# Optimization experiments

Measured on AMD Instinct MI355X. Metric: run time of the kernel, lower is better.

## Reference

```python
import jax, jax.numpy as jnp
import numpy as np


def setup_inputs() -> dict:
    key = jax.random.key(0)
    k1, k2 = jax.random.split(key)
    shape = (4096, 16384)  # d_model x d_ff weight matrix, 64M elements
    weight = jax.random.normal(k1, shape, dtype=jnp.float32)
    mask_weights = jax.random.normal(k2, shape, dtype=jnp.float32)
    return {"weight": weight, "mask_weights": mask_weights, "masking_percent": 0.5}


def reference(weight, mask_weights, masking_percent):
    # torch: topk(mask_weights.flat, k=int((1-p)*N), largest=False) -> zero those
    # positions in a clone of weight.
    flat_mask = mask_weights.reshape(-1)
    n = flat_mask.shape[0]
    k = int((1.0 - masking_percent) * n)  # static python int (p is a python float)
    # bottom-k of mask_weights == top-k of its negation
    _, bottomk_idx = jax.lax.top_k(-flat_mask, k)
    masked = weight.reshape(-1).at[bottomk_idx].set(0.0)
    return masked.reshape(weight.shape)
```

## Files before the change

kernel.cpp:

```cpp
#include <hip/hip_runtime.h>

#define HIST_BITS 12
#define NBINS (1 << HIST_BITS)
#define KEY_SHIFT (32 - HIST_BITS)
#define REP 4

typedef float fx4 __attribute__((ext_vector_type(4)));

struct Ctrl {
    long long k;
    long long r1;
    int b1;
    unsigned counter;
};

__device__ __forceinline__ unsigned fkey(float f) {
    unsigned u = __float_as_uint(f);
    return (u & 0x80000000u) ? ~u : (u | 0x80000000u);
}

__global__ void k_zero(unsigned* __restrict__ hist, Ctrl* __restrict__ ctrl) {
    int i = blockIdx.x * blockDim.x + threadIdx.x;
    if (i < NBINS) hist[i] = 0;
    if (i == 0) {
        ctrl->k = 0; ctrl->r1 = 0; ctrl->b1 = -1; ctrl->counter = 0;
    }
}

__global__ void __launch_bounds__(1024)
k_hist(const float* __restrict__ mask, long long n, unsigned* __restrict__ ghist) {
    __shared__ unsigned sh[NBINS * REP];
    for (int i = threadIdx.x; i < NBINS * REP; i += blockDim.x) sh[i] = 0;
    __syncthreads();

    const unsigned r = threadIdx.x & (REP - 1);
    const long long n4 = n >> 2;
    const fx4* m4 = (const fx4*)mask;
    const long long B = blockDim.x;
    const long long per = (n4 + gridDim.x - 1) / gridDim.x;
    const long long s0 = (long long)blockIdx.x * per;
    const long long e = (s0 + per < n4) ? s0 + per : n4;

    long long i = s0 + threadIdx.x;
    for (; i + 3 * B < e; i += 4 * B) {
        fx4 a = m4[i];
        fx4 b = m4[i + B];
        fx4 c = m4[i + 2 * B];
        fx4 d = m4[i + 3 * B];
        atomicAdd(&sh[(fkey(a.x) >> KEY_SHIFT) * REP + r], 1u);
        atomicAdd(&sh[(fkey(a.y) >> KEY_SHIFT) * REP + r], 1u);
        atomicAdd(&sh[(fkey(a.z) >> KEY_SHIFT) * REP + r], 1u);
        atomicAdd(&sh[(fkey(a.w) >> KEY_SHIFT) * REP + r], 1u);
        atomicAdd(&sh[(fkey(b.x) >> KEY_SHIFT) * REP + r], 1u);
        atomicAdd(&sh[(fkey(b.y) >> KEY_SHIFT) * REP + r], 1u);
        atomicAdd(&sh[(fkey(b.z) >> KEY_SHIFT) * REP + r], 1u);
        atomicAdd(&sh[(fkey(b.w) >> KEY_SHIFT) * REP + r], 1u);
        atomicAdd(&sh[(fkey(c.x) >> KEY_SHIFT) * REP + r], 1u);
        atomicAdd(&sh[(fkey(c.y) >> KEY_SHIFT) * REP + r], 1u);
        atomicAdd(&sh[(fkey(c.z) >> KEY_SHIFT) * REP + r], 1u);
        atomicAdd(&sh[(fkey(c.w) >> KEY_SHIFT) * REP + r], 1u);
        atomicAdd(&sh[(fkey(d.x) >> KEY_SHIFT) * REP + r], 1u);
        atomicAdd(&sh[(fkey(d.y) >> KEY_SHIFT) * REP + r], 1u);
        atomicAdd(&sh[(fkey(d.z) >> KEY_SHIFT) * REP + r], 1u);
        atomicAdd(&sh[(fkey(d.w) >> KEY_SHIFT) * REP + r], 1u);
    }
    for (; i < e; i += B) {
        fx4 a = m4[i];
        atomicAdd(&sh[(fkey(a.x) >> KEY_SHIFT) * REP + r], 1u);
        atomicAdd(&sh[(fkey(a.y) >> KEY_SHIFT) * REP + r], 1u);
        atomicAdd(&sh[(fkey(a.z) >> KEY_SHIFT) * REP + r], 1u);
        atomicAdd(&sh[(fkey(a.w) >> KEY_SHIFT) * REP + r], 1u);
    }
    if (blockIdx.x == 0 && threadIdx.x == 0) {
        for (long long t = n4 * 4; t < n; ++t)
            atomicAdd(&ghist[fkey(mask[t]) >> KEY_SHIFT], 1u);
    }
    __syncthreads();
    for (int b = threadIdx.x; b < NBINS; b += blockDim.x) {
        unsigned s = sh[b * REP] + sh[b * REP + 1] + sh[b * REP + 2] + sh[b * REP + 3];
        if (s) atomicAdd(&ghist[b], s);
    }
}

__global__ void k_scan(const unsigned* __restrict__ ghist, Ctrl* __restrict__ ctrl,
                       const float* __restrict__ p_ptr, long long n) {
    __shared__ long long part[256];
    __shared__ long long kk_sh;
    const int t = threadIdx.x;
    if (t == 0) {
        double p = (double)p_ptr[0];
        long long k = (long long)((1.0 - p) * (double)n);
        if (k < 0) k = 0;
        if (k > n) k = n;
        kk_sh = k;
        ctrl->k = k;
        ctrl->b1 = -1;
        ctrl->r1 = 0;
    }
    __syncthreads();
    const long long k = kk_sh;

    const int per = NBINS / 256;
    long long s = 0;
    for (int i = 0; i < per; ++i) s += (long long)ghist[t * per + i];
    part[t] = s;
    __syncthreads();
    for (int off = 1; off < 256; off <<= 1) {
        long long add = (t >= off) ? part[t - off] : 0;
        __syncthreads();
        part[t] += add;
        __syncthreads();
    }
    if (k >= 1) {
        long long incl = part[t];
        long long excl = incl - s;
        if (excl < k && k <= incl) {
            long long cum = excl;
            for (int i = 0; i < per; ++i) {
                long long c = (long long)ghist[t * per + i];
                if (cum < k && k <= cum + c) {
                    ctrl->b1 = t * per + i;
                    ctrl->r1 = k - cum;
                    break;
                }
                cum += c;
            }
        }
    }
}

__device__ __forceinline__ void cand4(unsigned k0, unsigned k1, unsigned k2, unsigned k3,
                                      unsigned base, unsigned b1u,
                                      Ctrl* ctrl, uint2* list, unsigned cap) {
    if ((k0 >> KEY_SHIFT) == b1u) { unsigned p = atomicAdd(&ctrl->counter, 1u); if (p < cap) list[p] = make_uint2(k0, base + 0); }
    if ((k1 >> KEY_SHIFT) == b1u) { unsigned p = atomicAdd(&ctrl->counter, 1u); if (p < cap) list[p] = make_uint2(k1, base + 1); }
    if ((k2 >> KEY_SHIFT) == b1u) { unsigned p = atomicAdd(&ctrl->counter, 1u); if (p < cap) list[p] = make_uint2(k2, base + 2); }
    if ((k3 >> KEY_SHIFT) == b1u) { unsigned p = atomicAdd(&ctrl->counter, 1u); if (p < cap) list[p] = make_uint2(k3, base + 3); }
}

__global__ void __launch_bounds__(256)
k_apply(const float* __restrict__ w, const float* __restrict__ mask,
        float* __restrict__ out, long long n,
        Ctrl* __restrict__ ctrl, uint2* __restrict__ list, unsigned cap) {
    const int b1 = ctrl->b1;
    const unsigned b1u = (unsigned)b1;
    const unsigned lo = (b1 <= 0) ? 0u : ((unsigned)b1 << KEY_SHIFT);
    const long long n4 = n >> 2;
    const fx4* m4 = (const fx4*)mask;
    const fx4* w4 = (const fx4*)w;
    fx4* o4 = (fx4*)out;
    const long long B = blockDim.x;
    const long long per = (n4 + gridDim.x - 1) / gridDim.x;
    const long long s0 = (long long)blockIdx.x * per;
    const long long e = (s0 + per < n4) ? s0 + per : n4;

    long long i = s0 + threadIdx.x;
    for (; i + 3 * B < e; i += 4 * B) {
        fx4 m0 = m4[i];
        fx4 m1 = m4[i + B];
        fx4 m2 = m4[i + 2 * B];
        fx4 m3 = m4[i + 3 * B];
        fx4 w0 = __builtin_nontemporal_load(&w4[i]);
        fx4 w1 = __builtin_nontemporal_load(&w4[i + B]);
        fx4 w2 = __builtin_nontemporal_load(&w4[i + 2 * B]);
        fx4 w3 = __builtin_nontemporal_load(&w4[i + 3 * B]);
        unsigned k00 = fkey(m0.x), k01 = fkey(m0.y), k02 = fkey(m0.z), k03 = fkey(m0.w);
        unsigned k10 = fkey(m1.x), k11 = fkey(m1.y), k12 = fkey(m1.z), k13 = fkey(m1.w);
        unsigned k20 = fkey(m2.x), k21 = fkey(m2.y), k22 = fkey(m2.z), k23 = fkey(m2.w);
        unsigned k30 = fkey(m3.x), k31 = fkey(m3.y), k32 = fkey(m3.z), k33 = fkey(m3.w);
        fx4 o0, o1, o2, o3;
        o0.x = (k00 >= lo) ? w0.x : 0.0f;  o0.y = (k01 >= lo) ? w0.y : 0.0f;
        o0.z = (k02 >= lo) ? w0.z : 0.0f;  o0.w = (k03 >= lo) ? w0.w : 0.0f;
        o1.x = (k10 >= lo) ? w1.x : 0.0f;  o1.y = (k11 >= lo) ? w1.y : 0.0f;
        o1.z = (k12 >= lo) ? w1.z : 0.0f;  o1.w = (k13 >= lo) ? w1.w : 0.0f;
        o2.x = (k20 >= lo) ? w2.x : 0.0f;  o2.y = (k21 >= lo) ? w2.y : 0.0f;
        o2.z = (k22 >= lo) ? w2.z : 0.0f;  o2.w = (k23 >= lo) ? w2.w : 0.0f;
        o3.x = (k30 >= lo) ? w3.x : 0.0f;  o3.y = (k31 >= lo) ? w3.y : 0.0f;
        o3.z = (k32 >= lo) ? w3.z : 0.0f;  o3.w = (k33 >= lo) ? w3.w : 0.0f;
        __builtin_nontemporal_store(o0, &o4[i]);
        __builtin_nontemporal_store(o1, &o4[i + B]);
        __builtin_nontemporal_store(o2, &o4[i + 2 * B]);
        __builtin_nontemporal_store(o3, &o4[i + 3 * B]);
        bool anyc = ((k00 >> KEY_SHIFT) == b1u) | ((k01 >> KEY_SHIFT) == b1u) |
                    ((k02 >> KEY_SHIFT) == b1u) | ((k03 >> KEY_SHIFT) == b1u) |
                    ((k10 >> KEY_SHIFT) == b1u) | ((k11 >> KEY_SHIFT) == b1u) |
                    ((k12 >> KEY_SHIFT) == b1u) | ((k13 >> KEY_SHIFT) == b1u) |
                    ((k20 >> KEY_SHIFT) == b1u) | ((k21 >> KEY_SHIFT) == b1u) |
                    ((k22 >> KEY_SHIFT) == b1u) | ((k23 >> KEY_SHIFT) == b1u) |
                    ((k30 >> KEY_SHIFT) == b1u) | ((k31 >> KEY_SHIFT) == b1u) |
                    ((k32 >> KEY_SHIFT) == b1u) | ((k33 >> KEY_SHIFT) == b1u);
        if (__any(anyc)) {
            cand4(k00, k01, k02, k03, (unsigned)(i * 4), b1u, ctrl, list, cap);
            cand4(k10, k11, k12, k13, (unsigned)((i + B) * 4), b1u, ctrl, list, cap);
            cand4(k20, k21, k22, k23, (unsigned)((i + 2 * B) * 4), b1u, ctrl, list, cap);
            cand4(k30, k31, k32, k33, (unsigned)((i + 3 * B) * 4), b1u, ctrl, list, cap);
        }
    }
    for (; i < e; i += B) {
        fx4 m0 = m4[i];
        fx4 w0 = __builtin_nontemporal_load(&w4[i]);
        unsigned k00 = fkey(m0.x), k01 = fkey(m0.y), k02 = fkey(m0.z), k03 = fkey(m0.w);
        fx4 o0;
        o0.x = (k00 >= lo) ? w0.x : 0.0f;  o0.y = (k01 >= lo) ? w0.y : 0.0f;
        o0.z = (k02 >= lo) ? w0.z : 0.0f;  o0.w = (k03 >= lo) ? w0.w : 0.0f;
        __builtin_nontemporal_store(o0, &o4[i]);
        bool anyc = ((k00 >> KEY_SHIFT) == b1u) | ((k01 >> KEY_SHIFT) == b1u) |
                    ((k02 >> KEY_SHIFT) == b1u) | ((k03 >> KEY_SHIFT) == b1u);
        if (__any(anyc))
            cand4(k00, k01, k02, k03, (unsigned)(i * 4), b1u, ctrl, list, cap);
    }
    if (blockIdx.x == 0 && threadIdx.x == 0) {
        for (long long t = n4 * 4; t < n; ++t) {
            unsigned key = fkey(mask[t]);
            out[t] = (key >= lo) ? w[t] : 0.0f;
            if ((key >> KEY_SHIFT) == b1u) {
                unsigned p = atomicAdd(&ctrl->counter, 1u);
                if (p < cap) list[p] = make_uint2(key, (unsigned)t);
            }
        }
    }
}

__global__ void k_fix(float* __restrict__ out, const Ctrl* __restrict__ ctrl,
                      const uint2* __restrict__ list, unsigned cap) {
    __shared__ uint2 ch[1024];
    unsigned nc = ctrl->counter;
    if (nc > cap) nc = cap;
    const long long r1 = ctrl->r1;
    if (ctrl->b1 < 0 || r1 <= 0) return;

    for (unsigned jb = 0; jb < nc; jb += blockDim.x) {
        unsigned j = jb + threadIdx.x;
        bool act = (j < nc);
        unsigned kj = 0, ij = 0;
        if (act) { uint2 e = list[j]; kj = e.x; ij = e.y; }
        long long rank = 0;
        for (unsigned cb = 0; cb < nc; cb += 1024) {
            unsigned mlen = nc - cb; if (mlen > 1024) mlen = 1024;
            for (unsigned u = threadIdx.x; u < mlen; u += blockDim.x) ch[u] = list[cb + u];
            __syncthreads();
            if (act) {
                for (unsigned u = 0; u < mlen; ++u) {
                    uint2 e = ch[u];
                    rank += (long long)((e.x < kj) || (e.x == kj && e.y < ij));
                }
            }
            __syncthreads();
        }
        if (act && rank < r1) out[ij] = 0.0f;
    }
}

extern "C" void kernel_launch(void* const* d_in, const int* in_sizes, int n_in,
                              void* d_out, int out_size, void* d_ws, size_t ws_size,
                              hipStream_t stream) {
    const float* weight = (const float*)d_in[0];
    const float* maskw  = (const float*)d_in[1];
    const float* pptr   = (const float*)d_in[2];
    float* out = (float*)d_out;
    const long long n = (long long)in_sizes[0];

    unsigned char* ws = (unsigned char*)d_ws;
    unsigned* hist = (unsigned*)ws;
    Ctrl* ctrl = (Ctrl*)(ws + 16384);
    uint2* list = (uint2*)(ws + 16416);
    size_t cap_sz = (ws_size > 16416) ? (ws_size - 16416) / sizeof(uint2) : 0;
    unsigned cap = (unsigned)(cap_sz > (size_t)(1u << 20) ? (1u << 20) : cap_sz);

    k_zero<<<(NBINS + 255) / 256, 256, 0, stream>>>(hist, ctrl);
    k_hist<<<512, 1024, 0, stream>>>(maskw, n, hist);
    k_scan<<<1, 256, 0, stream>>>(hist, ctrl, pptr, n);
    k_apply<<<2048, 256, 0, stream>>>(weight, maskw, out, n, ctrl, list, cap);
    k_fix<<<1, 256, 0, stream>>>(out, ctrl, list, cap);
}
```

Baseline: 185.1 us.

## Fuse histogram, scan and apply into one persistent kernel with grid barrier

Merges the histogram, threshold scan and masking kernels into a single 512x1024 kernel. The last-arriving block does the prefix scan while the other blocks spin on a flag, then every block applies the mask to the same slice it histogrammed. This is meant to cut kernel launch gaps and to make the second mask read come from cache. In exchange it depends on all blocks being co-resident, which risks a deadlock or timeout, and the single scanning block sits on the critical path while every other block waits.

Measured after the change: 381.6 us. 106% more time.

```diff
diff --git a/kernel.cpp b/kernel.cpp
--- a/kernel.cpp
+++ b/kernel.cpp
@@ -4,6 +4,8 @@
 #define NBINS (1 << HIST_BITS)
 #define KEY_SHIFT (32 - HIST_BITS)
 #define REP 4
+#define GRID 512
+#define BLK 1024
 
 typedef float fx4 __attribute__((ext_vector_type(4)));
 
@@ -12,6 +14,8 @@
     long long r1;
     int b1;
     unsigned counter;
+    unsigned arrive;
+    unsigned flag;
 };
 
 __device__ __forceinline__ unsigned fkey(float f) {
@@ -23,138 +27,144 @@
     int i = blockIdx.x * blockDim.x + threadIdx.x;
     if (i < NBINS) hist[i] = 0;
     if (i == 0) {
-        ctrl->k = 0; ctrl->r1 = 0; ctrl->b1 = -1; ctrl->counter = 0;
-    }
-}
-
-__global__ void __launch_bounds__(1024)
-k_hist(const float* __restrict__ mask, long long n, unsigned* __restrict__ ghist) {
+        ctrl->k = 0; ctrl->r1 = 0; ctrl->b1 = -1;
+        ctrl->counter = 0; ctrl->arrive = 0; ctrl->flag = 0;
+    }
+}
+
+__global__ void __launch_bounds__(BLK, 8)
+k_fused(const float* __restrict__ w, const float* __restrict__ mask,
+        float* __restrict__ out, long long n, const float* __restrict__ p_ptr,
+        unsigned* __restrict__ ghist, Ctrl* __restrict__ ctrl,
+        uint2* __restrict__ list, unsigned cap) {
     __shared__ unsigned sh[NBINS * REP];
-    for (int i = threadIdx.x; i < NBINS * REP; i += blockDim.x) sh[i] = 0;
-    __syncthreads();
-
-    const unsigned r = threadIdx.x & (REP - 1);
+    __shared__ int s_last;
+    __shared__ int sb1;
+
+    const int tid = threadIdx.x;
+    if (tid == 0) s_last = 0;
+    for (int i = tid; i < NBINS * REP; i += BLK) sh[i] = 0;
+    __syncthreads();
+
     const long long n4 = n >> 2;
     const fx4* m4 = (const fx4*)mask;
-    const long long B = blockDim.x;
+    const long long B = BLK;
     const long long per = (n4 + gridDim.x - 1) / gridDim.x;
     const long long s0 = (long long)blockIdx.x * per;
     const long long e = (s0 + per < n4) ? s0 + per : n4;
 
-    long long i = s0 + threadIdx.x;
-    for (; i + 3 * B < e; i += 4 * B) {
-        fx4 a = m4[i];
-        fx4 b = m4[i + B];
-        fx4 c = m4[i + 2 * B];
-        fx4 d = m4[i + 3 * B];
-        atomicAdd(&sh[(fkey(a.x) >> KEY_SHIFT) * REP + r], 1u);
-        atomicAdd(&sh[(fkey(a.y) >> KEY_SHIFT) * REP + r], 1u);
-        atomicAdd(&sh[(fkey(a.z) >> KEY_SHIFT) * REP + r], 1u);
-        atomicAdd(&sh[(fkey(a.w) >> KEY_SHIFT) * REP + r], 1u);
-        atomicAdd(&sh[(fkey(b.x) >> KEY_SHIFT) * REP + r], 1u);
-        atomicAdd(&sh[(fkey(b.y) >> KEY_SHIFT) * REP + r], 1u);
-        atomicAdd(&sh[(fkey(b.z) >> KEY_SHIFT) * REP + r], 1u);
-        atomicAdd(&sh[(fkey(b.w) >> KEY_SHIFT) * REP + r], 1u);
-        atomicAdd(&sh[(fkey(c.x) >> KEY_SHIFT) * REP + r], 1u);
-        atomicAdd(&sh[(fkey(c.y) >> KEY_SHIFT) * REP + r], 1u);
-        atomicAdd(&sh[(fkey(c.z) >> KEY_SHIFT) * REP + r], 1u);
-        atomicAdd(&sh[(fkey(c.w) >> KEY_SHIFT) * REP + r], 1u);
-        atomicAdd(&sh[(fkey(d.x) >> KEY_SHIFT) * REP + r], 1u);
-        atomicAdd(&sh[(fkey(d.y) >> KEY_SHIFT) * REP + r], 1u);
-        atomicAdd(&sh[(fkey(d.z) >> KEY_SHIFT) * REP + r], 1u);
-        atomicAdd(&sh[(fkey(d.w) >> KEY_SHIFT) * REP + r], 1u);
-    }
-    for (; i < e; i += B) {
-        fx4 a = m4[i];
-        atomicAdd(&sh[(fkey(a.x) >> KEY_SHIFT) * REP + r], 1u);
-        atomicAdd(&sh[(fkey(a.y) >> KEY_SHIFT) * REP + r], 1u);
-        atomicAdd(&sh[(fkey(a.z) >> KEY_SHIFT) * REP + r], 1u);
-        atomicAdd(&sh[(fkey(a.w) >> KEY_SHIFT) * REP + r], 1u);
-    }
-    if (blockIdx.x == 0 && threadIdx.x == 0) {
-        for (long long t = n4 * 4; t < n; ++t)
-            atomicAdd(&ghist[fkey(mask[t]) >> KEY_SHIFT], 1u);
-    }
-    __syncthreads();
-    for (int b = threadIdx.x; b < NBINS; b += blockDim.x) {
+    {
+        const unsigned r = tid & (REP - 1);
+        long long i = s0 + tid;
+        for (; i + 3 * B < e; i += 4 * B) {
+            fx4 a = m4[i];
+            fx4 b = m4[i + B];
+            fx4 c = m4[i + 2 * B];
+            fx4 d = m4[i + 3 * B];
+            atomicAdd(&sh[(fkey(a.x) >> KEY_SHIFT) * REP + r], 1u);
+            atomicAdd(&sh[(fkey(a.y) >> KEY_SHIFT) * REP + r], 1u);
+            atomicAdd(&sh[(fkey(a.z) >> KEY_SHIFT) * REP + r], 1u);
+            atomicAdd(&sh[(fkey(a.w) >> KEY_SHIFT) * REP + r], 1u);
+            atomicAdd(&sh[(fkey(b.x) >> KEY_SHIFT) * REP + r], 1u);
+            atomicAdd(&sh[(fkey(b.y) >> KEY_SHIFT) * REP + r], 1u);
+            atomicAdd(&sh[(fkey(b.z) >> KEY_SHIFT) * REP + r], 1u);
+            atomicAdd(&sh[(fkey(b.w) >> KEY_SHIFT) * REP + r], 1u);
+            atomicAdd(&sh[(fkey(c.x) >> KEY_SHIFT) * REP + r], 1u);
+            atomicAdd(&sh[(fkey(c.y) >> KEY_SHIFT) * REP + r], 1u);
+            atomicAdd(&sh[(fkey(c.z) >> KEY_SHIFT) * REP + r], 1u);
+            atomicAdd(&sh[(fkey(c.w) >> KEY_SHIFT) * REP + r], 1u);
+            atomicAdd(&sh[(fkey(d.x) >> KEY_SHIFT) * REP + r], 1u);
+            atomicAdd(&sh[(fkey(d.y) >> KEY_SHIFT) * REP + r], 1u);
+            atomicAdd(&sh[(fkey(d.z) >> KEY_SHIFT) * REP + r], 1u);
+            atomicAdd(&sh[(fkey(d.w) >> KEY_SHIFT) * REP + r], 1u);
+        }
+        for (; i < e; i += B) {
+            fx4 a = m4[i];
+            atomicAdd(&sh[(fkey(a.x) >> KEY_SHIFT) * REP + r], 1u);
+            atomicAdd(&sh[(fkey(a.y) >> KEY_SHIFT) * REP + r], 1u);
+            atomicAdd(&sh[(fkey(a.z) >> KEY_SHIFT) * REP + r], 1u);
+            atomicAdd(&sh[(fkey(a.w) >> KEY_SHIFT) * REP + r], 1u);
+        }
+        if (blockIdx.x == 0 && tid == 0) {
+            for (long long t = n4 * 4; t < n; ++t)
+                atomicAdd(&ghist[fkey(mask[t]) >> KEY_SHIFT], 1u);
+        }
+    }
+    __syncthreads();
+    for (int b = tid; b < NBINS; b += BLK) {
         unsigned s = sh[b * REP] + sh[b * REP + 1] + sh[b * REP + 2] + sh[b * REP + 3];
         if (s) atomicAdd(&ghist[b], s);
     }
-}
-
-__global__ void k_scan(const unsigned* __restrict__ ghist, Ctrl* __restrict__ ctrl,
-                       const float* __restrict__ p_ptr, long long n) {
-    __shared__ long long part[256];
-    __shared__ long long kk_sh;
-    const int t = threadIdx.x;
-    if (t == 0) {
+    __threadfence();
+    __syncthreads();
+
+    if (tid == 0) {
+        unsigned old = atomicAdd(&ctrl->arrive, 1u);
+        if (old == gridDim.x - 1) s_last = 1;
+    }
+    __syncthreads();
+
+    if (s_last) {
+        long long* part = (long long*)sh;
         double p = (double)p_ptr[0];
-        long long k = (long long)((1.0 - p) * (double)n);
-        if (k < 0) k = 0;
-        if (k > n) k = n;
-        kk_sh = k;
-        ctrl->k = k;
-        ctrl->b1 = -1;
-        ctrl->r1 = 0;
-    }
-    __syncthreads();
-    const long long k = kk_sh;
-
-    const int per = NBINS / 256;
-    long long s = 0;
-    for (int i = 0; i < per; ++i) s += (long long)ghist[t * per + i];
-    part[t] = s;
-    __syncthreads();
-    for (int off = 1; off < 256; off <<= 1) {
-        long long add = (t >= off) ? part[t - off] : 0;
+        long long kk = (long long)((1.0 - p) * (double)n);
+        if (kk < 0) kk = 0;
+        if (kk > n) kk = n;
+        const int pern = NBINS / BLK;
+        unsigned c0 = __hip_atomic_load(&ghist[tid * pern + 0], __ATOMIC_RELAXED, __HIP_MEMORY_SCOPE_AGENT);
+        unsigned c1 = __hip_atomic_load(&ghist[tid * pern + 1], __ATOMIC_RELAXED, __HIP_MEMORY_SCOPE_AGENT);
+        unsigned c2 = __hip_atomic_load(&ghist[tid * pern + 2], __ATOMIC_RELAXED, __HIP_MEMORY_SCOPE_AGENT);
+        unsigned c3 = __hip_atomic_load(&ghist[tid * pern + 3], __ATOMIC_RELAXED, __HIP_MEMORY_SCOPE_AGENT);
+        long long s = (long long)c0 + c1 + c2 + c3;
+        part[tid] = s;
         __syncthreads();
-        part[t] += add;
+        for (int off = 1; off < BLK; off <<= 1) {
+            long long add = (tid >= off) ? part[tid - off] : 0;
+            __syncthreads();
+            part[tid] += add;
+            __syncthreads();
+        }
+        if (kk >= 1) {
+            long long incl = part[tid];
+            long long excl = incl - s;
+            if (excl < kk && kk <= incl) {
+                long long cum = excl;
+                unsigned cs[4] = {c0, c1, c2, c3};
+                for (int i = 0; i < pern; ++i) {
+                    long long c = (long long)cs[i];
+                    if (cum < kk && kk <= cum + c) {
+                        __hip_atomic_store(&ctrl->b1, tid * pern + i, __ATOMIC_RELAXED, __HIP_MEMORY_SCOPE_AGENT);
+                        __hip_atomic_store(&ctrl->r1, kk - cum, __ATOMIC_RELAXED, __HIP_MEMORY_SCOPE_AGENT);
+                        break;
+                    }
+                    cum += c;
+                }
+            }
+        }
         __syncthreads();
-    }
-    if (k >= 1) {
-        long long incl = part[t];
-        long long excl = incl - s;
-        if (excl < k && k <= incl) {
-            long long cum = excl;
-            for (int i = 0; i < per; ++i) {
-                long long c = (long long)ghist[t * per + i];
-                if (cum < k && k <= cum + c) {
-                    ctrl->b1 = t * per + i;
-                    ctrl->r1 = k - cum;
-                    break;
-                }
-                cum += c;
-            }
-        }
-    }
-}
-
-__device__ __forceinline__ void cand4(unsigned k0, unsigned k1, unsigned k2, unsigned k3,
-                                      unsigned base, unsigned b1u,
-                                      Ctrl* ctrl, uint2* list, unsigned cap) {
-    if ((k0 >> KEY_SHIFT) == b1u) { unsigned p = atomicAdd(&ctrl->counter, 1u); if (p < cap) list[p] = make_uint2(k0, base + 0); }
-    if ((k1 >> KEY_SHIFT) == b1u) { unsigned p = atomicAdd(&ctrl->counter, 1u); if (p < cap) list[p] = make_uint2(k1, base + 1); }
-    if ((k2 >> KEY_SHIFT) == b1u) { unsigned p = atomicAdd(&ctrl->counter, 1u); if (p < cap) list[p] = make_uint2(k2, base + 2); }
-    if ((k3 >> KEY_SHIFT) == b1u) { unsigned p = atomicAdd(&ctrl->counter, 1u); if (p < cap) list[p] = make_uint2(k3, base + 3); }
-}
-
-__global__ void __launch_bounds__(256)
-k_apply(const float* __restrict__ w, const float* __restrict__ mask,
-        float* __restrict__ out, long long n,
-        Ctrl* __restrict__ ctrl, uint2* __restrict__ list, unsigned cap) {
-    const int b1 = ctrl->b1;
+        if (tid == 0) {
+            __threadfence();
+            __hip_atomic_store(&ctrl->flag, 1u, __ATOMIC_RELEASE, __HIP_MEMORY_SCOPE_AGENT);
+        }
+    }
+
+    if (tid == 0) {
+        int t = 0;
+        while (__hip_atomic_load(&ctrl->flag, __ATOMIC_ACQUIRE, __HIP_MEMORY_SCOPE_AGENT) == 0u) {
+            __builtin_amdgcn_s_sleep(32);
+            if (++t > 2000000) break;
+        }
+        sb1 = __hip_atomic_load(&ctrl->b1, __ATOMIC_RELAXED, __HIP_MEMORY_SCOPE_AGENT);
+    }
+    __syncthreads();
+    const int b1 = sb1;
+
     const unsigned b1u = (unsigned)b1;
     const unsigned lo = (b1 <= 0) ? 0u : ((unsigned)b1 << KEY_SHIFT);
-    const long long n4 = n >> 2;
-    const fx4* m4 = (const fx4*)mask;
     const fx4* w4 = (const fx4*)w;
     fx4* o4 = (fx4*)out;
-    const long long B = blockDim.x;
-    const long long per = (n4 + gridDim.x - 1) / gridDim.x;
-    const long long s0 = (long long)blockIdx.x * per;
-    const long long e = (s0 + per < n4) ? s0 + per : n4;
-
-    long long i = s0 + threadIdx.x;
+
+    long long i = s0 + tid;
     for (; i + 3 * B < e; i += 4 * B) {
         fx4 m0 = m4[i];
         fx4 m1 = m4[i + B];
@@ -190,10 +200,14 @@
                     ((k30 >> KEY_SHIFT) == b1u) | ((k31 >> KEY_SHIFT) == b1u) |
                     ((k32 >> KEY_SHIFT) == b1u) | ((k33 >> KEY_SHIFT) == b1u);
         if (__any(anyc)) {
-            cand4(k00, k01, k02, k03, (unsigned)(i * 4), b1u, ctrl, list, cap);
-            cand4(k10, k11, k12, k13, (unsigned)((i + B) * 4), b1u, ctrl, list, cap);
-            cand4(k20, k21, k22, k23, (unsigned)((i + 2 * B) * 4), b1u, ctrl, list, cap);
-            cand4(k30, k31, k32, k33, (unsigned)((i + 3 * B) * 4), b1u, ctrl, list, cap);
+            unsigned ks[16] = {k00,k01,k02,k03,k10,k11,k12,k13,k20,k21,k22,k23,k30,k31,k32,k33};
+            long long bases[4] = {i, i + B, i + 2 * B, i + 3 * B};
+            for (int q = 0; q < 4; ++q)
+                for (int j = 0; j < 4; ++j)
+                    if ((ks[q * 4 + j] >> KEY_SHIFT) == b1u) {
+                        unsigned p = atomicAdd(&ctrl->counter, 1u);
+                        if (p < cap) list[p] = make_uint2(ks[q * 4 + j], (unsigned)(bases[q] * 4 + j));
+                    }
         }
     }
     for (; i < e; i += B) {
@@ -206,10 +220,16 @@
         __builtin_nontemporal_store(o0, &o4[i]);
         bool anyc = ((k00 >> KEY_SHIFT) == b1u) | ((k01 >> KEY_SHIFT) == b1u) |
                     ((k02 >> KEY_SHIFT) == b1u) | ((k03 >> KEY_SHIFT) == b1u);
-        if (__any(anyc))
-            cand4(k00, k01, k02, k03, (unsigned)(i * 4), b1u, ctrl, list, cap);
-    }
-    if (blockIdx.x == 0 && threadIdx.x == 0) {
+        if (__any(anyc)) {
+            unsigned ks[4] = {k00, k01, k02, k03};
+            for (int j = 0; j < 4; ++j)
+                if ((ks[j] >> KEY_SHIFT) == b1u) {
+                    unsigned p = atomicAdd(&ctrl->counter, 1u);
+                    if (p < cap) list[p] = make_uint2(ks[j], (unsigned)(i * 4 + j));
+                }
+        }
+    }
+    if (blockIdx.x == 0 && tid == 0) {
         for (long long t = n4 * 4; t < n; ++t) {
             unsigned key = fkey(mask[t]);
             out[t] = (key >= lo) ? w[t] : 0.0f;
@@ -263,13 +283,11 @@
     unsigned char* ws = (unsigned char*)d_ws;
     unsigned* hist = (unsigned*)ws;
     Ctrl* ctrl = (Ctrl*)(ws + 16384);
-    uint2* list = (uint2*)(ws + 16416);
-    size_t cap_sz = (ws_size > 16416) ? (ws_size - 16416) / sizeof(uint2) : 0;
+    uint2* list = (uint2*)(ws + 16448);
+    size_t cap_sz = (ws_size > 16448) ? (ws_size - 16448) / sizeof(uint2) : 0;
     unsigned cap = (unsigned)(cap_sz > (size_t)(1u << 20) ? (1u << 20) : cap_sz);
 
     k_zero<<<(NBINS + 255) / 256, 256, 0, stream>>>(hist, ctrl);
-    k_hist<<<512, 1024, 0, stream>>>(maskw, n, hist);
-    k_scan<<<1, 256, 0, stream>>>(hist, ctrl, pptr, n);
-    k_apply<<<2048, 256, 0, stream>>>(weight, maskw, out, n, ctrl, list, cap);
-    k_fix<<<1, 256, 0, stream>>>(out, ctrl, list, cap);
-}
+    k_fused<<<GRID, BLK, 0, stream>>>(weight, maskw, out, n, pptr, hist, ctrl, list, cap);
+    k_fix<<<1, 1024, 0, stream>>>(out, ctrl, list, cap);
+}
```
